# Kernel optimization log

Measured on AMD Instinct MI355X. Metric: run time of the kernel, lower is better.

Reference implementation:

```python
import jax, jax.numpy as jnp
import numpy as np

SL, BS, HS = 2048, 4, 1024
FFN, E, TOPK = 4096, 8, 2
T = SL * BS


def setup_inputs() -> dict:
    key = jax.random.key(0)
    k1, k2, k3, k4, k5 = jax.random.split(key, 5)
    x = jax.random.normal(k1, (SL, BS, HS), dtype=jnp.float32)
    expert_weights = jax.random.uniform(k2, (T, TOPK), dtype=jnp.float32)
    w1 = jax.random.normal(k3, (E, HS, FFN), dtype=jnp.float32) * (HS ** -0.5)
    w2 = jax.random.normal(k4, (E, FFN, HS), dtype=jnp.float32) * (FFN ** -0.5)
    expert_indices = jax.random.randint(k5, (T, TOPK), 0, E, dtype=jnp.int32)
    return {"x": x, "expert_weights": expert_weights, "w1": w1, "w2": w2,
            "expert_indices": expert_indices}


def reference(x, expert_weights, w1, w2, expert_indices):
    """Dropless MoE: dispatch each token to its top_k experts, run the
    per-expert MLP (x @ W1 -> gelu -> @ W2), combine weighted copies.

    Equivalent math to megablocks sort/gather -> grouped GEMM -> scatter:
    each (token, k) row is processed by exactly expert_indices[t, k]'s MLP
    and the results are summed back per token with expert_weights.
    """
    in_shape = x.shape
    hs = x.shape[-1]
    xf = x.reshape(-1, hs)                      # [T, H]
    top_k = expert_indices.shape[-1]
    eids = expert_indices.reshape(-1)           # [T*top_k]
    # gather: replicate each token top_k times (row j <-> token j // top_k)
    x_rep = jnp.repeat(xf, top_k, axis=0)       # [T*top_k, H]

    def per_expert(acc, ewb):
        e, w1_e, w2_e = ewb
        h = jax.nn.gelu(x_rep @ w1_e)           # [T*top_k, F]
        y = h @ w2_e                            # [T*top_k, H]
        mask = (eids == e).astype(x.dtype)[:, None]
        return acc + mask * y, None

    n_exp = w1.shape[0]
    acc0 = jnp.zeros_like(x_rep)
    out_flat, _ = jax.lax.scan(per_expert, acc0, (jnp.arange(n_exp), w1, w2))
    # scatter-combine: weighted sum of the top_k expert outputs per token
    w_flat = expert_weights.reshape(-1, 1)      # [T*top_k, 1]
    out = (w_flat * out_flat).reshape(-1, top_k, hs).sum(axis=1)
    return out.reshape(in_shape)
```

## Files before the change

kernel.cpp:

```cpp
#include <hip/hip_runtime.h>
#include <hip/hip_bf16.h>
#include <stdint.h>
#include <stddef.h>

#define SLEN 2048
#define BSZ  4
#define HSD  1024
#define FFND 4096
#define NEXP 8
#define NTOP 2
#define NTOK (SLEN*BSZ)
#define NROW (NTOK*NTOP)
#define NRP  (NROW + NEXP*256)
#define MAXT (NROW/256 + NEXP)

typedef __hip_bfloat16 bf16;
typedef __attribute__((ext_vector_type(8))) __bf16 b8v;
typedef __attribute__((ext_vector_type(4))) float f4v;

static constexpr size_t OFF_BLOCKHIST = 0;
static constexpr size_t OFF_BLOCKBASE = 2048;
static constexpr size_t OFF_SCHED_E   = 4096;
static constexpr size_t OFF_SCHED_R   = 4736;
static constexpr size_t OFF_NTILES    = 5376;
static constexpr size_t OFF_STOK      = 8192;
static constexpr size_t OFF_SWT       = OFF_STOK + 73728;
static constexpr size_t OFF_SLOT      = OFF_SWT + 73728;
static constexpr size_t OFF_XB        = 221184;
static constexpr size_t OFF_W1T       = OFF_XB  + (size_t)NTOK*HSD*2;
static constexpr size_t OFF_W2T       = OFF_W1T + (size_t)NEXP*FFND*HSD*2;
static constexpr size_t OFF_H         = OFF_W2T + (size_t)NEXP*HSD*FFND*2;
static constexpr size_t WS_NEED       = OFF_H   + (size_t)NRP*FFND*2;
static constexpr size_t OFF_YP        = OFF_XB;

__device__ __forceinline__ void gload_lds16(const void* g, void* l) {
  __builtin_amdgcn_global_load_lds(
      (const __attribute__((address_space(1))) unsigned int*)g,
      (__attribute__((address_space(3))) unsigned int*)l, 16, 0, 0);
}

__device__ __forceinline__ f4v mfma16(b8v a, b8v b, f4v c) {
  return __builtin_amdgcn_mfma_f32_16x16x32_bf16(a, b, c, 0, 0, 0);
}

__device__ __forceinline__ float gelu_tanh(float x) {
  float u = 0.7978845608028654f * x * (1.0f + 0.044715f * x * x);
  float e = __expf(2.0f * u);
  float t = 1.0f - 2.0f / (e + 1.0f);
  return 0.5f * x * (1.0f + t);
}

__global__ void moe_hist(const int* __restrict__ eidx, int* __restrict__ blockhist) {
  __shared__ int h[NEXP];
  int tid = threadIdx.x;
  if (tid < NEXP) h[tid] = 0;
  __syncthreads();
  int gid = blockIdx.x * 256 + tid;
  atomicAdd(&h[eidx[gid] & 7], 1);
  __syncthreads();
  if (tid < NEXP) blockhist[blockIdx.x * NEXP + tid] = h[tid];
}

__global__ void moe_plan(const int* __restrict__ blockhist, int* __restrict__ blockbase,
                         int* __restrict__ sched_e, int* __restrict__ sched_r,
                         int* __restrict__ ntiles,
                         int* __restrict__ stok, float* __restrict__ swt) {
  int tid = threadIdx.x;
  for (int i = tid; i < NRP; i += 256) { stok[i] = 0; swt[i] = 0.0f; }
  __syncthreads();
  if (tid == 0) {
    int cnt[NEXP], off[NEXP];
    for (int e = 0; e < NEXP; ++e) {
      int c = 0;
      for (int b = 0; b < 64; ++b) c += blockhist[b * NEXP + e];
      cnt[e] = c;
    }
    int run = 0, it = 0;
    for (int e = 0; e < NEXP; ++e) {
      off[e] = run;
      int nt = (cnt[e] + 255) >> 8;
      for (int j = 0; j < nt; ++j) { sched_e[it] = e; sched_r[it] = run + j * 256; ++it; }
      run += nt << 8;
    }
    *ntiles = it;
    for (int e = 0; e < NEXP; ++e) {
      int r = off[e];
      for (int b = 0; b < 64; ++b) { blockbase[b * NEXP + e] = r; r += blockhist[b * NEXP + e]; }
    }
  }
}

__global__ void moe_scatter(const int* __restrict__ eidx, const float* __restrict__ ew,
                            const int* __restrict__ blockbase,
                            int* __restrict__ stok, float* __restrict__ swt,
                            int* __restrict__ slot) {
  __shared__ int cur[NEXP];
  int tid = threadIdx.x;
  if (tid < NEXP) cur[tid] = blockbase[blockIdx.x * NEXP + tid];
  __syncthreads();
  int gid = blockIdx.x * 256 + tid;
  int e = eidx[gid] & 7;
  int pos = atomicAdd(&cur[e], 1);
  stok[pos] = gid >> 1;
  swt[pos]  = ew[gid];
  slot[gid] = pos;
}

__global__ void conv_x(const float* __restrict__ x, bf16* __restrict__ xb) {
  int gid = blockIdx.x * 256 + threadIdx.x;
  float4 v = ((const float4*)x)[gid];
  alignas(8) bf16 o[4];
  o[0] = __float2bfloat16(v.x); o[1] = __float2bfloat16(v.y);
  o[2] = __float2bfloat16(v.z); o[3] = __float2bfloat16(v.w);
  ((ushort4*)xb)[gid] = *(const ushort4*)o;
}

__global__ void transpose_conv(const float* __restrict__ src, bf16* __restrict__ dst,
                               int R, int C) {
  __shared__ float tile[32][65];
  int e = blockIdx.z;
  const float* s = src + (size_t)e * R * C;
  uint* d = (uint*)((ushort*)dst + (size_t)e * R * C);
  int c0 = blockIdx.x * 32, r0 = blockIdx.y * 64;
  int tx = threadIdx.x, ty = threadIdx.y;
  #pragma unroll
  for (int j = 0; j < 64; j += 8)
    tile[tx][ty + j] = s[(size_t)(r0 + ty + j) * C + (c0 + tx)];
  __syncthreads();
  #pragma unroll
  for (int j = 0; j < 32; j += 8) {
    int c = ty + j;
    alignas(4) bf16 p[2];
    p[0] = __float2bfloat16(tile[c][tx * 2]);
    p[1] = __float2bfloat16(tile[c][tx * 2 + 1]);
    d[(((size_t)(c0 + c) * R + r0) >> 1) + tx] = *(const uint*)p;
  }
}

template<int KDIM, int NDIM, int NSPLIT, bool GATHER, int ACT>
__global__ __launch_bounds__(512, 2)
void moe_gemm(const bf16* __restrict__ A, const bf16* __restrict__ B,
              bf16* __restrict__ OutBase,
              const int* __restrict__ stok,
              const int* __restrict__ sched_e, const int* __restrict__ sched_r,
              const int* __restrict__ ntiles) {
  constexpr int BM = 256, BN = 256, BK = 64;
  constexpr int BUFS = (BM + BN) * BK;
  constexpr int KT = KDIM / BK / NSPLIT;
  constexpr int JT = KT / 2;

  int rt = blockIdx.y;
  if (rt >= *ntiles) return;
  const int tid  = threadIdx.x;
  const int lane = tid & 63;
  const int wid  = tid >> 6;
  const int wm = wid & 1, wn = wid >> 1;
  const int e    = sched_e[rt];
  const int row0 = sched_r[rt];
  const int n0   = blockIdx.x * BN;
  const int z    = blockIdx.z;
  const int kbase = z * (KDIM / NSPLIT);
  bf16* Out = OutBase + (size_t)z * NRP * NDIM;

  __shared__ short lds[2 * BUFS];

  const int l15  = lane & 15;
  const int quad = lane >> 4;
  const int xor7 = l15 & 7;
  const ushort* Aus  = (const ushort*)A;
  const ushort* Bexp = (const ushort*)B + (size_t)e * NDIM * KDIM;

  const int rsub  = lane >> 3;
  const int kgsrc = (lane & 7) ^ rsub;
  const ushort* aP[2][2];
  const ushort* bP[2][2];
  #pragma unroll
  for (int h = 0; h < 2; ++h)
    #pragma unroll
    for (int q = 0; q < 2; ++q) {
      int xr = 128 * h + 8 * (2 * wid + q) + rsub;
      int grow = GATHER ? stok[row0 + xr] : (row0 + xr);
      aP[h][q] = Aus  + (size_t)grow * KDIM + kbase + kgsrc * 8;
      bP[h][q] = Bexp + (size_t)(n0 + xr) * KDIM + kbase + kgsrc * 8;
    }

  auto SA = [&](int b, int h, int T) {
    #pragma unroll
    for (int q = 0; q < 2; ++q)
      gload_lds16(aP[h][q] + T * 64, lds + b * BUFS + h * 8192 + (2 * wid + q) * 512);
  };
  auto SB = [&](int b, int h, int T) {
    #pragma unroll
    for (int q = 0; q < 2; ++q)
      gload_lds16(bP[h][q] + T * 64, lds + b * BUFS + BM * BK + h * 8192 + (2 * wid + q) * 512);
  };

  const int goff0 = (quad ^ xor7) << 3;
  const int goff1 = ((4 + quad) ^ xor7) << 3;
  const int mbase = (wm * 128 + l15) * 64;
  const int nbase = BM * BK + (wn * 64 + l15) * 64;

  f4v acc[8][4];
  #pragma unroll
  for (int mt = 0; mt < 8; ++mt)
    #pragma unroll
    for (int nt = 0; nt < 4; ++nt) acc[mt][nt] = (f4v)0.0f;

  b8v aF[2][4], bF0[2][2], bF1[2][2];

  auto LDA = [&](int b, int qm) {
    const short* base = lds + b * BUFS + mbase + qm * 4096;
    #pragma unroll
    for (int t = 0; t < 4; ++t) {
      aF[0][t] = *(const b8v*)(base + t * 1024 + goff0);
      aF[1][t] = *(const b8v*)(base + t * 1024 + goff1);
    }
  };
  auto LDB = [&](int b, int qn, b8v (&bF)[2][2]) {
    const short* base = lds + b * BUFS + nbase + qn * 2048;
    #pragma unroll
    for (int u = 0; u < 2; ++u) {
      bF[0][u] = *(const b8v*)(base + u * 1024 + goff0);
      bF[1][u] = *(const b8v*)(base + u * 1024 + goff1);
    }
  };
  auto MM = [&](int qm, int qn, b8v (&bF)[2][2]) {
    __builtin_amdgcn_s_setprio(1);
    #pragma unroll
    for (int s = 0; s < 2; ++s)
      #pragma unroll
      for (int t = 0; t < 4; ++t)
        #pragma unroll
        for (int u = 0; u < 2; ++u)
          acc[qm * 4 + t][qn * 2 + u] = mfma16(aF[s][t], bF[s][u], acc[qm * 4 + t][qn * 2 + u]);
    __builtin_amdgcn_s_setprio(0);
  };
  auto BAR = [&] {
    asm volatile("" ::: "memory");
    __builtin_amdgcn_s_barrier();
    asm volatile("" ::: "memory");
  };

  SB(0, 0, 0); SB(0, 1, 0); SA(0, 0, 0); SA(0, 1, 0);
  SB(1, 0, 1); SB(1, 1, 1);
  asm volatile("s_waitcnt vmcnt(4)" ::: "memory");
  __builtin_amdgcn_s_barrier();
  asm volatile("" ::: "memory");

  #pragma unroll 1
  for (int j = 0; j < JT; ++j) {
    const int t1 = 2 * j + 1, t2 = 2 * j + 2, t3 = 2 * j + 3;
    const bool more = (j + 1 < JT);
    LDA(0, 0); LDB(0, 0, bF0);
    SA(1, 0, t1);
    BAR(); MM(0, 0, bF0); BAR();
    LDB(0, 1, bF1);
    SA(1, 1, t1);
    BAR(); MM(0, 1, bF1); BAR();
    LDA(0, 1);
    if (more) SB(0, 0, t2);
    BAR(); MM(1, 1, bF1); BAR();
    if (more) SB(0, 1, t2);
    BAR(); MM(1, 0, bF0);
    if (more) asm volatile("s_waitcnt vmcnt(4)" ::: "memory");
    else      asm volatile("s_waitcnt vmcnt(0)" ::: "memory");
    BAR();
    LDA(1, 0); LDB(1, 0, bF0);
    if (more) SA(0, 0, t2);
    BAR(); MM(0, 0, bF0); BAR();
    LDB(1, 1, bF1);
    if (more) SA(0, 1, t2);
    BAR(); MM(0, 1, bF1); BAR();
    LDA(1, 1);
    if (more) SB(1, 0, t3);
    BAR(); MM(1, 1, bF1); BAR();
    if (more) SB(1, 1, t3);
    BAR(); MM(1, 0, bF0);
    asm volatile("s_waitcnt vmcnt(4)" ::: "memory");
    BAR();
  }

  #pragma unroll
  for (int mt = 0; mt < 8; ++mt)
    #pragma unroll
    for (int nt = 0; nt < 4; ++nt) {
      f4v v = acc[mt][nt];
      #pragma unroll
      for (int r = 0; r < 4; ++r) {
        int m = row0 + wm * 128 + mt * 16 + quad * 4 + r;
        int n = n0   + wn * 64  + nt * 16 + l15;
        float o = (ACT == 0) ? gelu_tanh(v[r]) : v[r];
        Out[(size_t)m * NDIM + n] = __float2bfloat16(o);
      }
    }
}

__global__ void moe_combine(const bf16* __restrict__ Yp, const float* __restrict__ swt,
                            const int* __restrict__ slot, float* __restrict__ out) {
  int gid = blockIdx.x * 256 + threadIdx.x;
  int t  = gid >> 7;
  int ho = (gid & 127) << 3;
  int s0 = slot[t * 2], s1 = slot[t * 2 + 1];
  float w0 = swt[s0], w1 = swt[s1];
  const __bf16* Y0 = (const __bf16*)Yp;
  const __bf16* Y1 = Y0 + (size_t)NRP * HSD;
  b8v a0 = *(const b8v*)(Y0 + (size_t)s0 * HSD + ho);
  b8v a1 = *(const b8v*)(Y1 + (size_t)s0 * HSD + ho);
  b8v b0 = *(const b8v*)(Y0 + (size_t)s1 * HSD + ho);
  b8v b1 = *(const b8v*)(Y1 + (size_t)s1 * HSD + ho);
  float o[8];
  #pragma unroll
  for (int i = 0; i < 8; ++i)
    o[i] = w0 * ((float)a0[i] + (float)a1[i]) + w1 * ((float)b0[i] + (float)b1[i]);
  float4* op = (float4*)(out + (size_t)t * HSD + ho);
  op[0] = make_float4(o[0], o[1], o[2], o[3]);
  op[1] = make_float4(o[4], o[5], o[6], o[7]);
}

extern "C" void kernel_launch(void* const* d_in, const int* in_sizes, int n_in,
                              void* d_out, int out_size, void* d_ws, size_t ws_size,
                              hipStream_t stream) {
  const float* x    = (const float*)d_in[0];
  const float* ew   = (const float*)d_in[1];
  const float* w1   = (const float*)d_in[2];
  const float* w2   = (const float*)d_in[3];
  const int*   eidx = (const int*)d_in[4];
  float* out = (float*)d_out;
  char* ws = (char*)d_ws;

  if (ws_size < WS_NEED) {
    hipMemsetAsync(d_out, 0x7F, 8, stream);
    return;
  }

  int*   blockhist = (int*)(ws + OFF_BLOCKHIST);
  int*   blockbase = (int*)(ws + OFF_BLOCKBASE);
  int*   sched_e   = (int*)(ws + OFF_SCHED_E);
  int*   sched_r   = (int*)(ws + OFF_SCHED_R);
  int*   ntiles    = (int*)(ws + OFF_NTILES);
  int*   stok      = (int*)(ws + OFF_STOK);
  float* swt       = (float*)(ws + OFF_SWT);
  int*   slot      = (int*)(ws + OFF_SLOT);
  bf16*  xb        = (bf16*)(ws + OFF_XB);
  bf16*  w1t       = (bf16*)(ws + OFF_W1T);
  bf16*  w2t       = (bf16*)(ws + OFF_W2T);
  bf16*  Hbuf      = (bf16*)(ws + OFF_H);
  bf16*  Ypart     = (bf16*)(ws + OFF_YP);

  moe_hist<<<64, 256, 0, stream>>>(eidx, blockhist);
  moe_plan<<<1, 256, 0, stream>>>(blockhist, blockbase, sched_e, sched_r, ntiles, stok, swt);
  moe_scatter<<<64, 256, 0, stream>>>(eidx, ew, blockbase, stok, swt, slot);

  conv_x<<<(NTOK * HSD / 4) / 256, 256, 0, stream>>>(x, xb);
  transpose_conv<<<dim3(FFND / 32, HSD / 64, NEXP), dim3(32, 8), 0, stream>>>(w1, w1t, HSD, FFND);
  transpose_conv<<<dim3(HSD / 32, FFND / 64, NEXP), dim3(32, 8), 0, stream>>>(w2, w2t, FFND, HSD);

  moe_gemm<HSD, FFND, 1, true, 0><<<dim3(FFND / 256, MAXT, 1), 512, 0, stream>>>(
      xb, w1t, Hbuf, stok, sched_e, sched_r, ntiles);
  moe_gemm<FFND, HSD, 2, false, 1><<<dim3(HSD / 256, MAXT, 2), 512, 0, stream>>>(
      Hbuf, w2t, Ypart, stok, sched_e, sched_r, ntiles);

  moe_combine<<<NTOK * HSD / 8 / 256, 256, 0, stream>>>(Ypart, swt, slot, out);
}
```

Before: 734.7 us.

## Fuse prep kernels, parallelize plan, and add XCD-aware workgroup swizzle to GEMMs

Merges the x conversion, both weight transposes and the expert histogram into one prep launch selected by block index. The plan kernel now loads the histogram into shared memory and computes per-expert counts and bases with eight threads instead of one. Both grouped GEMMs remap the flat workgroup id so that consecutive logical tiles land on the same XCD, aiming for better L2 reuse of shared A/B tiles. The aim is to cut launch overhead and serial work; the swizzle may change tail behaviour when empty tiles exit early.

```diff
diff --git a/kernel.cpp b/kernel.cpp
--- a/kernel.cpp
+++ b/kernel.cpp
@@ -50,31 +50,86 @@
   return 0.5f * x * (1.0f + t);
 }
 
-__global__ void moe_hist(const int* __restrict__ eidx, int* __restrict__ blockhist) {
-  __shared__ int h[NEXP];
+#define NB_CONV (NTOK*HSD/4/256)
+#define NB_W1   (NEXP*(HSD/64)*(FFND/32))
+#define NB_W2   (NEXP*(FFND/64)*(HSD/32))
+#define NB_HIST 64
+#define NB_PREP (NB_CONV + NB_W1 + NB_W2 + NB_HIST)
+
+template<int R, int C>
+__device__ __forceinline__ void transpose_body(const float* __restrict__ src,
+                                               bf16* __restrict__ dst,
+                                               int l, int tid) {
+  __shared__ float tile[32][65];
+  constexpr int CT = C / 32, RT = R / 64;
+  int e   = l / (CT * RT);
+  int rem = l - e * (CT * RT);
+  int by  = rem / CT, bx = rem % CT;
+  const float* s = src + (size_t)e * R * C;
+  uint* d = (uint*)((ushort*)dst + (size_t)e * R * C);
+  int c0 = bx * 32, r0 = by * 64;
+  int tx = tid & 31, ty = tid >> 5;
+  #pragma unroll
+  for (int j = 0; j < 64; j += 8)
+    tile[tx][ty + j] = s[(size_t)(r0 + ty + j) * C + (c0 + tx)];
+  __syncthreads();
+  #pragma unroll
+  for (int j = 0; j < 32; j += 8) {
+    int c = ty + j;
+    alignas(4) bf16 p[2];
+    p[0] = __float2bfloat16(tile[c][tx * 2]);
+    p[1] = __float2bfloat16(tile[c][tx * 2 + 1]);
+    d[(((size_t)(c0 + c) * R + r0) >> 1) + tx] = *(const uint*)p;
+  }
+}
+
+__global__ void moe_prep(const float* __restrict__ x, bf16* __restrict__ xb,
+                         const float* __restrict__ w1, bf16* __restrict__ w1t,
+                         const float* __restrict__ w2, bf16* __restrict__ w2t,
+                         const int* __restrict__ eidx, int* __restrict__ blockhist) {
+  int bid = blockIdx.x;
   int tid = threadIdx.x;
-  if (tid < NEXP) h[tid] = 0;
-  __syncthreads();
-  int gid = blockIdx.x * 256 + tid;
-  atomicAdd(&h[eidx[gid] & 7], 1);
-  __syncthreads();
-  if (tid < NEXP) blockhist[blockIdx.x * NEXP + tid] = h[tid];
+  if (bid < NB_CONV) {
+    int gid = bid * 256 + tid;
+    float4 v = ((const float4*)x)[gid];
+    alignas(8) bf16 o[4];
+    o[0] = __float2bfloat16(v.x); o[1] = __float2bfloat16(v.y);
+    o[2] = __float2bfloat16(v.z); o[3] = __float2bfloat16(v.w);
+    ((ushort4*)xb)[gid] = *(const ushort4*)o;
+  } else if (bid < NB_CONV + NB_W1) {
+    transpose_body<HSD, FFND>(w1, w1t, bid - NB_CONV, tid);
+  } else if (bid < NB_CONV + NB_W1 + NB_W2) {
+    transpose_body<FFND, HSD>(w2, w2t, bid - NB_CONV - NB_W1, tid);
+  } else {
+    __shared__ int h[NEXP];
+    int b = bid - NB_CONV - NB_W1 - NB_W2;
+    if (tid < NEXP) h[tid] = 0;
+    __syncthreads();
+    int gid = b * 256 + tid;
+    atomicAdd(&h[eidx[gid] & 7], 1);
+    __syncthreads();
+    if (tid < NEXP) blockhist[b * NEXP + tid] = h[tid];
+  }
 }
 
 __global__ void moe_plan(const int* __restrict__ blockhist, int* __restrict__ blockbase,
                          int* __restrict__ sched_e, int* __restrict__ sched_r,
                          int* __restrict__ ntiles,
                          int* __restrict__ stok, float* __restrict__ swt) {
+  __shared__ int h[64 * NEXP];
+  __shared__ int cnt[NEXP], off[NEXP];
   int tid = threadIdx.x;
   for (int i = tid; i < NRP; i += 256) { stok[i] = 0; swt[i] = 0.0f; }
+  for (int i = tid; i < 64 * NEXP; i += 256) h[i] = blockhist[i];
+  __syncthreads();
+  if (tid < NEXP) {
+    int c = 0;
+    #pragma unroll
+    for (int b = 0; b < 64; ++b) c += h[b * NEXP + tid];
+    cnt[tid] = c;
+  }
   __syncthreads();
   if (tid == 0) {
-    int cnt[NEXP], off[NEXP];
-    for (int e = 0; e < NEXP; ++e) {
-      int c = 0;
-      for (int b = 0; b < 64; ++b) c += blockhist[b * NEXP + e];
-      cnt[e] = c;
-    }
     int run = 0, it = 0;
     for (int e = 0; e < NEXP; ++e) {
       off[e] = run;
@@ -83,10 +138,12 @@
       run += nt << 8;
     }
     *ntiles = it;
-    for (int e = 0; e < NEXP; ++e) {
-      int r = off[e];
-      for (int b = 0; b < 64; ++b) { blockbase[b * NEXP + e] = r; r += blockhist[b * NEXP + e]; }
-    }
+  }
+  __syncthreads();
+  if (tid < NEXP) {
+    int r = off[tid];
+    #pragma unroll
+    for (int b = 0; b < 64; ++b) { blockbase[b * NEXP + tid] = r; r += h[b * NEXP + tid]; }
   }
 }
 
@@ -106,38 +163,7 @@
   slot[gid] = pos;
 }
 
-__global__ void conv_x(const float* __restrict__ x, bf16* __restrict__ xb) {
-  int gid = blockIdx.x * 256 + threadIdx.x;
-  float4 v = ((const float4*)x)[gid];
-  alignas(8) bf16 o[4];
-  o[0] = __float2bfloat16(v.x); o[1] = __float2bfloat16(v.y);
-  o[2] = __float2bfloat16(v.z); o[3] = __float2bfloat16(v.w);
-  ((ushort4*)xb)[gid] = *(const ushort4*)o;
-}
-
-__global__ void transpose_conv(const float* __restrict__ src, bf16* __restrict__ dst,
-                               int R, int C) {
-  __shared__ float tile[32][65];
-  int e = blockIdx.z;
-  const float* s = src + (size_t)e * R * C;
-  uint* d = (uint*)((ushort*)dst + (size_t)e * R * C);
-  int c0 = blockIdx.x * 32, r0 = blockIdx.y * 64;
-  int tx = threadIdx.x, ty = threadIdx.y;
-  #pragma unroll
-  for (int j = 0; j < 64; j += 8)
-    tile[tx][ty + j] = s[(size_t)(r0 + ty + j) * C + (c0 + tx)];
-  __syncthreads();
-  #pragma unroll
-  for (int j = 0; j < 32; j += 8) {
-    int c = ty + j;
-    alignas(4) bf16 p[2];
-    p[0] = __float2bfloat16(tile[c][tx * 2]);
-    p[1] = __float2bfloat16(tile[c][tx * 2 + 1]);
-    d[(((size_t)(c0 + c) * R + r0) >> 1) + tx] = *(const uint*)p;
-  }
-}
-
-template<int KDIM, int NDIM, int NSPLIT, bool GATHER, int ACT>
+template<int KDIM, int NDIM, int NSPLIT, bool GATHER, int ACT, int GX, int NWG>
 __global__ __launch_bounds__(512, 2)
 void moe_gemm(const bf16* __restrict__ A, const bf16* __restrict__ B,
               bf16* __restrict__ OutBase,
@@ -148,8 +174,16 @@
   constexpr int BUFS = (BM + BN) * BK;
   constexpr int KT = KDIM / BK / NSPLIT;
   constexpr int JT = KT / 2;
-
-  int rt = blockIdx.y;
+  static_assert(NWG % 8 == 0, "XCD swizzle needs nwg % 8 == 0");
+  constexpr unsigned Q = NWG / 8;
+
+  unsigned flat = (blockIdx.z * MAXT + blockIdx.y) * GX + blockIdx.x;
+  unsigned nf = (flat & 7) * Q + (flat >> 3);
+  const int bx = nf % GX;
+  unsigned t2 = nf / GX;
+  const int rt = t2 % MAXT;
+  const int z  = t2 / MAXT;
+
   if (rt >= *ntiles) return;
   const int tid  = threadIdx.x;
   const int lane = tid & 63;
@@ -157,8 +191,7 @@
   const int wm = wid & 1, wn = wid >> 1;
   const int e    = sched_e[rt];
   const int row0 = sched_r[rt];
-  const int n0   = blockIdx.x * BN;
-  const int z    = blockIdx.z;
+  const int n0   = bx * BN;
   const int kbase = z * (KDIM / NSPLIT);
   bf16* Out = OutBase + (size_t)z * NRP * NDIM;
 
@@ -249,7 +282,7 @@
 
   #pragma unroll 1
   for (int j = 0; j < JT; ++j) {
-    const int t1 = 2 * j + 1, t2 = 2 * j + 2, t3 = 2 * j + 3;
+    const int t1 = 2 * j + 1, t2i = 2 * j + 2, t3 = 2 * j + 3;
     const bool more = (j + 1 < JT);
     LDA(0, 0); LDB(0, 0, bF0);
     SA(1, 0, t1);
@@ -258,18 +291,18 @@
     SA(1, 1, t1);
     BAR(); MM(0, 1, bF1); BAR();
     LDA(0, 1);
-    if (more) SB(0, 0, t2);
+    if (more) SB(0, 0, t2i);
     BAR(); MM(1, 1, bF1); BAR();
-    if (more) SB(0, 1, t2);
+    if (more) SB(0, 1, t2i);
     BAR(); MM(1, 0, bF0);
     if (more) asm volatile("s_waitcnt vmcnt(4)" ::: "memory");
     else      asm volatile("s_waitcnt vmcnt(0)" ::: "memory");
     BAR();
     LDA(1, 0); LDB(1, 0, bF0);
-    if (more) SA(0, 0, t2);
+    if (more) SA(0, 0, t2i);
     BAR(); MM(0, 0, bF0); BAR();
     LDB(1, 1, bF1);
-    if (more) SA(0, 1, t2);
+    if (more) SA(0, 1, t2i);
     BAR(); MM(0, 1, bF1); BAR();
     LDA(1, 1);
     if (more) SB(1, 0, t3);
@@ -347,17 +380,15 @@
   bf16*  Hbuf      = (bf16*)(ws + OFF_H);
   bf16*  Ypart     = (bf16*)(ws + OFF_YP);
 
-  moe_hist<<<64, 256, 0, stream>>>(eidx, blockhist);
+  moe_prep<<<NB_PREP, 256, 0, stream>>>(x, xb, w1, w1t, w2, w2t, eidx, blockhist);
   moe_plan<<<1, 256, 0, stream>>>(blockhist, blockbase, sched_e, sched_r, ntiles, stok, swt);
   moe_scatter<<<64, 256, 0, stream>>>(eidx, ew, blockbase, stok, swt, slot);
 
-  conv_x<<<(NTOK * HSD / 4) / 256, 256, 0, stream>>>(x, xb);
-  transpose_conv<<<dim3(FFND / 32, HSD / 64, NEXP), dim3(32, 8), 0, stream>>>(w1, w1t, HSD, FFND);
-  transpose_conv<<<dim3(HSD / 32, FFND / 64, NEXP), dim3(32, 8), 0, stream>>>(w2, w2t, FFND, HSD);
-
-  moe_gemm<HSD, FFND, 1, true, 0><<<dim3(FFND / 256, MAXT, 1), 512, 0, stream>>>(
+  moe_gemm<HSD, FFND, 1, true, 0, FFND/256, (FFND/256)*MAXT>
+      <<<dim3(FFND / 256, MAXT, 1), 512, 0, stream>>>(
       xb, w1t, Hbuf, stok, sched_e, sched_r, ntiles);
-  moe_gemm<FFND, HSD, 2, false, 1><<<dim3(HSD / 256, MAXT, 2), 512, 0, stream>>>(
+  moe_gemm<FFND, HSD, 2, false, 1, HSD/256, (HSD/256)*MAXT*2>
+      <<<dim3(HSD / 256, MAXT, 2), 512, 0, stream>>>(
       Hbuf, w2t, Ypart, stok, sched_e, sched_r, ntiles);
 
   moe_combine<<<NTOK * HSD / 8 / 256, 256, 0, stream>>>(Ypart, swt, slot, out);
```

Result: faster. 701.7 us (-4.5%).
